# Kernel optimization log

Measured on AMD Instinct MI355X. Metric: run time of the kernel, lower is better.

## Reference

```python
import jax, jax.numpy as jnp
import numpy as np

B, T, E, H, K, V = 256, 200, 100, 128, 13, 50000


def run_lstm(x, W, U, b, reverse=False):
    """Keras LSTM with activation=relu, recurrent_activation=sigmoid.
    x: [B,T,E]; W: [E,4H]; U: [H,4H]; b: [4H]. Gate order: i, f, g, o.
    Returns hidden states [B,T,H] (time-aligned for both directions)."""
    Bn = x.shape[0]
    Hn = U.shape[0]
    xw = jnp.einsum('bte,eg->btg', x, W) + b  # precompute input projections [B,T,4H]

    def step(carry, xw_t):
        h, c = carry
        z = xw_t + h @ U
        i, f, g, o = jnp.split(z, 4, axis=-1)
        i = jax.nn.sigmoid(i)
        f = jax.nn.sigmoid(f)
        g = jax.nn.relu(g)          # activation=relu (non-cuDNN path in TF)
        c = f * c + i * g
        h = o * jax.nn.relu(c)      # output activation also relu
        return (h, c), h

    init = (jnp.zeros((Bn, Hn), x.dtype), jnp.zeros((Bn, Hn), x.dtype))
    _, hs = jax.lax.scan(step, init, jnp.swapaxes(xw, 0, 1), reverse=reverse)
    return jnp.swapaxes(hs, 0, 1)


def crf_log_likelihood(logits, labels, lens, trans):
    """tfa.text.crf_log_likelihood: score(labels) - logZ, masked by seq lens."""
    Bn, Tn, Kn = logits.shape
    t_idx = jnp.arange(Tn)
    mask = t_idx[None, :] < lens[:, None]  # [B,T]
    # unary score
    unary = jnp.take_along_axis(logits, labels[..., None], axis=-1)[..., 0]
    u_score = jnp.sum(jnp.where(mask, unary, 0.0), axis=-1)
    # transition score
    pair = trans[labels[:, :-1], labels[:, 1:]]  # [B,T-1]
    pmask = t_idx[None, 1:] < lens[:, None]
    b_score = jnp.sum(jnp.where(pmask, pair, 0.0), axis=-1)
    # forward algorithm (log-space DP over time, masked updates)
    def step(alpha, inp):
        logit_t, valid = inp  # [B,K], [B]
        new = jax.nn.logsumexp(alpha[:, :, None] + trans[None], axis=1) + logit_t
        alpha = jnp.where(valid[:, None], new, alpha)
        return alpha, None

    alpha0 = logits[:, 0, :]
    xs = (jnp.swapaxes(logits[:, 1:, :], 0, 1), jnp.swapaxes(mask[:, 1:], 0, 1))
    alpha, _ = jax.lax.scan(step, alpha0, xs)
    logZ = jax.nn.logsumexp(alpha, axis=-1)
    return u_score + b_score - logZ


def setup_inputs() -> dict:
    key = jax.random.key(0)
    ks = jax.random.split(key, 12)
    s = lambda k, shape, sc: jax.random.normal(k, shape, jnp.float32) * sc
    return {
        'text': jax.random.randint(ks[0], (B, T), 0, V).astype(jnp.int32),
        'labels': jax.random.randint(ks[1], (B, T), 0, K).astype(jnp.int32),
        'emb': s(ks[2], (V, E), 0.1),
        'Wf': s(ks[3], (E, 4 * H), 0.05),
        'Uf': s(ks[4], (H, 4 * H), 0.05),
        'bf': jnp.zeros((4 * H,), jnp.float32),
        'Wb': s(ks[5], (E, 4 * H), 0.05),
        'Ub': s(ks[6], (H, 4 * H), 0.05),
        'bb': jnp.zeros((4 * H,), jnp.float32),
        'Wd': s(ks[7], (2 * H, K), 0.05),
        'bd': jnp.zeros((K,), jnp.float32),
        'trans': jax.random.uniform(ks[8], (K, K), jnp.float32),
    }


def reference(text, labels, emb, Wf, Uf, bf, Wb, Ub, bb, Wd, bd, trans):
    lens = jnp.sum((text != 0).astype(jnp.int32), axis=-1)  # [B]
    x = emb[text]                      # embedding lookup [B,T,E]
    # dropout is identity in eval mode
    h_fwd = run_lstm(x, Wf, Uf, bf, reverse=False)
    h_bwd = run_lstm(x, Wb, Ub, bb, reverse=True)
    h = jnp.concatenate([h_fwd, h_bwd], axis=-1)  # [B,T,2H]
    logits = jax.nn.softmax(h @ Wd + bd, axis=-1)  # Dense(softmax), per source
    log_likelihood = crf_log_likelihood(logits, labels, lens, trans)
    return logits, lens, log_likelihood
```

## Files before the change

### kernel.cpp

```cpp
#include <hip/hip_runtime.h>
#include <hip/hip_bf16.h>

#define Bn 256
#define Tn 200
#define En 100
#define Hn 128
#define Kn 13
#define G4 512
#define BT 51200

typedef __attribute__((ext_vector_type(8))) __bf16 bf8_t;
typedef __attribute__((ext_vector_type(4))) float f4_t;

__device__ __forceinline__ unsigned short f2bf(float f) {
  unsigned int u = __float_as_uint(f);
  u = (u + 0x7FFFu + ((u >> 16) & 1u)) >> 16;
  return (unsigned short)u;
}
__device__ __forceinline__ float bf2f(unsigned short s) {
  return __uint_as_float(((unsigned int)s) << 16);
}
__device__ __forceinline__ float sigm(float x) { return 1.f / (1.f + __expf(-x)); }

__device__ __forceinline__ void bar_lgkm() {
  asm volatile("s_waitcnt lgkmcnt(0)" ::: "memory");
  __builtin_amdgcn_s_barrier();
  __builtin_amdgcn_sched_barrier(0);
}

__device__ __forceinline__ int gperm(int n) {
  return ((n >> 4) & 3) * 128 + ((n >> 6) << 4) + (n & 15);
}

__global__ __launch_bounds__(256) void k_prep(const int* __restrict__ text,
                                              const float* __restrict__ Wf,
                                              const float* __restrict__ Wb,
                                              const float* __restrict__ Uf,
                                              const float* __restrict__ Ub,
                                              unsigned short* __restrict__ wt,
                                              unsigned short* __restrict__ ut,
                                              int* __restrict__ lens_i,
                                              float* __restrict__ out_lens) {
  int bx = blockIdx.x;
  if (bx < 1024) {
    int idx = bx * 256 + threadIdx.x;
    int half = idx >> 17;
    int rem = idx & 131071;
    int dir = rem >> 16;
    int nk = rem & 65535;
    int n = nk >> 7, k = nk & 127;
    int mc = gperm(n);
    if (half == 0) {
      const float* W = dir ? Wb : Wf;
      wt[rem] = f2bf((k < En) ? W[k * G4 + mc] : 0.f);
    } else {
      const float* U = dir ? Ub : Uf;
      ut[rem] = f2bf(U[k * G4 + mc]);
    }
  } else {
    int wi = threadIdx.x >> 6, lane = threadIdx.x & 63;
    int b = (bx - 1024) * 4 + wi;
    int cnt = 0;
    for (int t = lane; t < Tn; t += 64) cnt += (text[b * Tn + t] != 0);
    for (int off = 32; off; off >>= 1) cnt += __shfl_down(cnt, off);
    if (lane == 0) { lens_i[b] = cnt; out_lens[b] = (float)cnt; }
  }
}

#define FR16(M) M(0,0) M(0,1) M(0,2) M(0,3) M(1,0) M(1,1) M(1,2) M(1,3) \
                M(2,0) M(2,1) M(2,2) M(2,3) M(3,0) M(3,1) M(3,2) M(3,3)

__global__ __attribute__((amdgpu_flat_work_group_size(512, 512),
                          amdgpu_waves_per_eu(1, 2)))
void k_scan(const int* __restrict__ text,
            const float* __restrict__ emb,
            const unsigned short* __restrict__ wt,
            const unsigned short* __restrict__ ut,
            const float* __restrict__ biasf,
            const float* __restrict__ biasb,
            unsigned short* __restrict__ hf,
            unsigned short* __restrict__ hb) {
  int blk = blockIdx.x;
  int dir = blk >> 6;
  int bg = blk & 63;
  int b0 = bg * 4;
  int tid = threadIdx.x;
  int w = tid >> 6, l = tid & 63;
  int lr = l & 15, lg = l >> 4;
  int jj = w * 16 + lr;
  const unsigned short* ut_d = ut + (size_t)dir * (G4 * 128);
  const unsigned short* wt_d = wt + (size_t)dir * (G4 * 128);
  const float* bias = dir ? biasb : biasf;
  unsigned short* hout = dir ? hb : hf;
  int t0 = dir ? (Tn - 1) : 0;
  int dt = dir ? -1 : 1;

#define LOADUB(nt, kk) \
  bf8_t ub_##nt##_##kk = *(const bf8_t*)(ut_d + (size_t)(w * 64 + (nt) * 16 + lr) * 128 + (kk) * 32 + lg * 8); \
  asm volatile("" : "+a"(ub_##nt##_##kk));
  FR16(LOADUB)
#undef LOADUB
#define LOADWB(nt, kk) \
  bf8_t wb_##nt##_##kk = *(const bf8_t*)(wt_d + (size_t)(w * 64 + (nt) * 16 + lr) * 128 + (kk) * 32 + lg * 8); \
  asm volatile("" : "+a"(wb_##nt##_##kk));
  FR16(LOADWB)
#undef LOADWB

  __shared__ __align__(16) char lds_all[16384 + Tn * 4 * 4];
  char* lbase = lds_all;
  int* tl = (int*)(lds_all + 16384);
  for (int i = tid; i < 4096; i += 512) ((unsigned int*)lds_all)[i] = 0;
  #pragma unroll
  for (int r = 0; r < 4; r++)
    if (tid < Tn) tl[r * Tn + tid] = text[(size_t)(b0 + r) * Tn + tid];

  float bn0 = bias[gperm(w * 64 +  0 + lr)];
  float bn1 = bias[gperm(w * 64 + 16 + lr)];
  float bn2 = bias[gperm(w * 64 + 32 + lr)];
  float bn3 = bias[gperm(w * 64 + 48 + lr)];
  f4_t bv0 = {bn0, bn0, bn0, bn0};
  f4_t bv1 = {bn1, bn1, bn1, bn1};
  f4_t bv2 = {bn2, bn2, bn2, bn2};
  f4_t bv3 = {bn3, bn3, bn3, bn3};
  f4_t z4 = {0.f, 0.f, 0.f, 0.f};

  int xrow = tid >> 7;
  int xcol = tid & 127;
  bool xon = (xcol < En);
  float v0 = 0.f, vA = 0.f, vB = 0.f;
  {
    const int* trow = text + (size_t)(b0 + xrow) * Tn;
    int k0 = trow[t0], k1 = trow[t0 + dt], k2 = trow[t0 + 2 * dt];
    if (xon) {
      v0 = emb[(size_t)k0 * En + xcol];
      vA = emb[(size_t)k1 * En + xcol];
      vB = emb[(size_t)k2 * En + xcol];
    }
  }

  int rb0 = (lr * 256 +   0 + lg * 16) ^ ((lr & 7) << 4);
  int rb1 = (lr * 256 +  64 + lg * 16) ^ ((lr & 7) << 4);
  int rb2 = (lr * 256 + 128 + lg * 16) ^ ((lr & 7) << 4);
  int rb3 = (lr * 256 + 192 + lg * 16) ^ ((lr & 7) << 4);
  int xb0 = 8192 + rb0, xb1 = 8192 + rb1, xb2 = 8192 + rb2, xb3 = 8192 + rb3;
  int wbh = (((lg * 4) * 256 + jj * 2) ^ (((lg * 4) & 7) << 4)) + 4096;
  int wbx = 8192 + (((xrow * 4) * 256 + xcol * 2) ^ (((xrow * 4) & 7) << 4));

  unsigned short* hp = hout + ((size_t)t0 * Bn + b0 + lg) * 128 + jj;
  const long long hstep = (long long)dt * Bn * 128;

  __syncthreads();
  *(unsigned short*)(lbase + wbx) = f2bf(v0);
  wbx ^= 4096;
  float c0 = 0.f;
  __syncthreads();

#define MFU(nt, kk) accU##nt = __builtin_amdgcn_mfma_f32_16x16x32_bf16(af##kk, ub_##nt##_##kk, accU##nt, 0, 0, 0);
#define MFW(nt, kk) accW##nt = __builtin_amdgcn_mfma_f32_16x16x32_bf16(ax##kk, wb_##nt##_##kk, accW##nt, 0, 0, 0);

  int t = t0;
  for (int tt = 0; tt < Tn; tt++) {
    *(unsigned short*)(lbase + wbx) = f2bf(vA);
    vA = vB;
    int tc = t + 3 * dt;
    tc = tc < 0 ? 0 : (tc > Tn - 1 ? Tn - 1 : tc);
    int tokN = tl[xrow * Tn + tc];
    vB = 0.f;
    if (xon) vB = emb[(size_t)tokN * En + xcol];
    bf8_t af0 = *(const bf8_t*)(lbase + rb0);
    bf8_t af1 = *(const bf8_t*)(lbase + rb1);
    bf8_t af2 = *(const bf8_t*)(lbase + rb2);
    bf8_t af3 = *(const bf8_t*)(lbase + rb3);
    bf8_t ax0 = *(const bf8_t*)(lbase + xb0);
    bf8_t ax1 = *(const bf8_t*)(lbase + xb1);
    bf8_t ax2 = *(const bf8_t*)(lbase + xb2);
    bf8_t ax3 = *(const bf8_t*)(lbase + xb3);
    f4_t accU0 = bv0, accU1 = bv1, accU2 = bv2, accU3 = bv3;
    f4_t accW0 = z4, accW1 = z4, accW2 = z4, accW3 = z4;
    MFU(0,0) MFU(1,0) MFU(2,0) MFU(3,0)
    MFW(0,0) MFW(1,0) MFW(2,0) MFW(3,0)
    MFU(0,1) MFU(1,1) MFU(2,1) MFU(3,1)
    MFW(0,1) MFW(1,1) MFW(2,1) MFW(3,1)
    MFU(0,2) MFU(1,2) MFU(2,2) MFU(3,2)
    MFW(0,2) MFW(1,2) MFW(2,2) MFW(3,2)
    MFU(0,3) MFU(1,3) MFU(2,3) MFU(3,3)
    MFW(0,3) MFW(1,3) MFW(2,3) MFW(3,3)
    float zi = accU0[0] + accW0[0];
    float zf = accU1[0] + accW1[0];
    float zg = accU2[0] + accW2[0];
    float zo = accU3[0] + accW3[0];
    float ig = sigm(zi);
    float fg = sigm(zf);
    float gg = fmaxf(zg, 0.f);
    c0 = fmaf(fg, c0, ig * gg);
    unsigned short hs2 = f2bf(sigm(zo) * fmaxf(c0, 0.f));
    *(unsigned short*)(lbase + wbh) = hs2;
    bar_lgkm();
    hp[0] = hs2;
    rb0 ^= 4096; rb1 ^= 4096; rb2 ^= 4096; rb3 ^= 4096;
    xb0 ^= 4096; xb1 ^= 4096; xb2 ^= 4096; xb3 ^= 4096;
    wbh ^= 4096; wbx ^= 4096;
    hp += hstep;
    t += dt;
  }
#undef MFU
#undef MFW
}

__global__ __launch_bounds__(128) void k_logits(const unsigned short* __restrict__ hf,
                                                const unsigned short* __restrict__ hb,
                                                const float* __restrict__ Wd,
                                                const float* __restrict__ bd,
                                                float* __restrict__ out) {
  __shared__ unsigned short hs[128 * 256];
  int tid = threadIdx.x;
  size_t row0 = (size_t)blockIdx.x * 128;
  #pragma unroll
  for (int it = 0; it < 16; it++) {
    int idx = it * 128 + tid;
    int r = idx >> 4, c = idx & 15;
    bf8_t vf = *(const bf8_t*)(hf + (row0 + r) * 128 + c * 8);
    bf8_t vb = *(const bf8_t*)(hb + (row0 + r) * 128 + c * 8);
    int byte = (r * 512 + c * 16) ^ ((r & 7) << 4);
    *(bf8_t*)((char*)hs + byte) = vf;
    int byte2 = (r * 512 + 256 + c * 16) ^ ((r & 7) << 4);
    *(bf8_t*)((char*)hs + byte2) = vb;
  }
  __syncthreads();
  float acc[Kn];
  #pragma unroll
  for (int jj = 0; jj < Kn; jj++) acc[jj] = bd[jj];
  int r = tid;
  #pragma unroll 4
  for (int c = 0; c < 32; c++) {
    int byte = (r * 512 + c * 16) ^ ((r & 7) << 4);
    bf8_t v = *(const bf8_t*)((const char*)hs + byte);
    #pragma unroll
    for (int e = 0; e < 8; e++) {
      float h = (float)v[e];
      int k = c * 8 + e;
      #pragma unroll
      for (int jj = 0; jj < Kn; jj++)
        acc[jj] = fmaf(h, Wd[k * Kn + jj], acc[jj]);
    }
  }
  float m = acc[0];
  #pragma unroll
  for (int jj = 1; jj < Kn; jj++) m = fmaxf(m, acc[jj]);
  float s = 0.f;
  #pragma unroll
  for (int jj = 0; jj < Kn; jj++) { acc[jj] = __expf(acc[jj] - m); s += acc[jj]; }
  float inv = 1.f / s;
  int rg = (int)row0 + tid;
  int b = rg & 255, t = rg >> 8;
  float* op = out + ((size_t)b * Tn + t) * Kn;
  #pragma unroll
  for (int jj = 0; jj < Kn; jj++) op[jj] = acc[jj] * inv;
}

__global__ __launch_bounds__(64) void k_crf(const float* __restrict__ logits,
                                            const int* __restrict__ labels,
                                            const int* __restrict__ lens_i,
                                            const float* __restrict__ trans,
                                            float* __restrict__ out_ll) {
  int b = blockIdx.x, lane = threadIdx.x;
  int len = lens_i[b];
  const float* lg = logits + (size_t)b * Tn * Kn;
  const int* lab = labels + (size_t)b * Tn;
  float sc = 0.f;
  for (int t = lane; t < Tn; t += 64) {
    if (t < len) {
      sc += lg[t * Kn + lab[t]];
      if (t >= 1) sc += trans[lab[t - 1] * Kn + lab[t]];
    }
  }
  for (int off = 32; off; off >>= 1) sc += __shfl_down(sc, off);
  bool act = lane < Kn;
  int jl = act ? lane : 0;
  float etr[Kn];
  #pragma unroll
  for (int i = 0; i < Kn; i++) etr[i] = __expf(trans[i * Kn + jl]);
  float a = act ? lg[jl] : -INFINITY;
  float lgv = (len > 1) ? lg[Kn + jl] : 0.f;
  for (int t = 1; t < len; t++) {
    float lgn = (t + 1 < len) ? lg[(t + 1) * Kn + jl] : 0.f;
    float m = a;
    for (int off = 8; off; off >>= 1) m = fmaxf(m, __shfl_xor(m, off, 16));
    float ea = __expf(a - m);
    float s = 0.f;
    #pragma unroll
    for (int i = 0; i < Kn; i++) s = fmaf(__shfl(ea, i), etr[i], s);
    float anew = m + __logf(s) + lgv;
    if (act) a = anew;
    lgv = lgn;
  }
  float m2 = a;
  for (int off = 8; off; off >>= 1) m2 = fmaxf(m2, __shfl_xor(m2, off, 16));
  float ea2 = act ? __expf(a - m2) : 0.f;
  float ssum = ea2;
  for (int off = 8; off; off >>= 1) ssum += __shfl_xor(ssum, off, 16);
  float logZ = m2 + __logf(ssum);
  if (lane == 0) out_ll[b] = sc - logZ;
}

extern "C" void kernel_launch(void* const* d_in, const int* in_sizes, int n_in,
                              void* d_out, int out_size, void* d_ws, size_t ws_size,
                              hipStream_t stream) {
  const int* text = (const int*)d_in[0];
  const int* labels = (const int*)d_in[1];
  const float* emb = (const float*)d_in[2];
  const float* Wf = (const float*)d_in[3];
  const float* Uf = (const float*)d_in[4];
  const float* bf_ = (const float*)d_in[5];
  const float* Wb = (const float*)d_in[6];
  const float* Ub = (const float*)d_in[7];
  const float* bb_ = (const float*)d_in[8];
  const float* Wd = (const float*)d_in[9];
  const float* bd = (const float*)d_in[10];
  const float* trans = (const float*)d_in[11];
  (void)in_sizes; (void)n_in; (void)out_size; (void)ws_size;

  float* out = (float*)d_out;
  float* out_logits = out;
  float* out_lens = out + (size_t)BT * Kn;
  float* out_ll = out_lens + Bn;

  char* ws = (char*)d_ws;
  size_t o = 0;
  int* lens_i = (int*)(ws + o);                o += 1024;
  unsigned short* wt = (unsigned short*)(ws + o);  o += (size_t)2 * G4 * 128 * 2;
  unsigned short* ut = (unsigned short*)(ws + o);  o += (size_t)2 * G4 * 128 * 2;
  unsigned short* hfb = (unsigned short*)(ws + o); o += (size_t)BT * Hn * 2;
  unsigned short* hbb = (unsigned short*)(ws + o); o += (size_t)BT * Hn * 2;

  hipLaunchKernelGGL(k_prep, dim3(1088), dim3(256), 0, stream,
                     text, Wf, Wb, Uf, Ub, wt, ut, lens_i, out_lens);
  hipLaunchKernelGGL(k_scan, dim3(128), dim3(512), 0, stream,
                     text, emb, wt, ut, bf_, bb_, hfb, hbb);
  hipLaunchKernelGGL(k_logits, dim3(400), dim3(128), 0, stream, hfb, hbb, Wd, bd, out_logits);
  hipLaunchKernelGGL(k_crf, dim3(Bn), dim3(64), 0, stream, out_logits, labels, lens_i, trans, out_ll);
}
```

Baseline: 319.2 us.

## Software-pipeline LSTM input projection one timestep ahead of the recurrence

The recurrent loop now computes the input-projection MFMAs (x·W plus bias) for the next timestep after the current step's h·U MFMAs, using two ping-ponged accumulator sets. The current step's gates depend only on the 16 recurrent MFMAs seeded with the precomputed projection. A prologue stages two embedding timesteps and computes the first projection, the x staging area moves to a separate LDS offset, and the loop is unrolled by two. The aim is to shorten the serial dependency chain per step and let the projection MFMAs overlap the gate math, at the cost of more accumulator registers.

```diff
diff --git a/kernel.cpp b/kernel.cpp
--- a/kernel.cpp
+++ b/kernel.cpp
@@ -122,19 +122,19 @@
   f4_t bv1 = {bn1, bn1, bn1, bn1};
   f4_t bv2 = {bn2, bn2, bn2, bn2};
   f4_t bv3 = {bn3, bn3, bn3, bn3};
-  f4_t z4 = {0.f, 0.f, 0.f, 0.f};
 
   int xrow = tid >> 7;
   int xcol = tid & 127;
   bool xon = (xcol < En);
-  float v0 = 0.f, vA = 0.f, vB = 0.f;
+  float v0 = 0.f, v1 = 0.f, vA = 0.f, vB = 0.f;
   {
     const int* trow = text + (size_t)(b0 + xrow) * Tn;
-    int k0 = trow[t0], k1 = trow[t0 + dt], k2 = trow[t0 + 2 * dt];
+    int k0 = trow[t0], k1 = trow[t0 + dt], k2 = trow[t0 + 2 * dt], k3 = trow[t0 + 3 * dt];
     if (xon) {
       v0 = emb[(size_t)k0 * En + xcol];
-      vA = emb[(size_t)k1 * En + xcol];
-      vB = emb[(size_t)k2 * En + xcol];
+      v1 = emb[(size_t)k1 * En + xcol];
+      vA = emb[(size_t)k2 * En + xcol];
+      vB = emb[(size_t)k3 * En + xcol];
     }
   }
 
@@ -142,69 +142,104 @@
   int rb1 = (lr * 256 +  64 + lg * 16) ^ ((lr & 7) << 4);
   int rb2 = (lr * 256 + 128 + lg * 16) ^ ((lr & 7) << 4);
   int rb3 = (lr * 256 + 192 + lg * 16) ^ ((lr & 7) << 4);
-  int xb0 = 8192 + rb0, xb1 = 8192 + rb1, xb2 = 8192 + rb2, xb3 = 8192 + rb3;
+  int xb0 = 12288 + rb0, xb1 = 12288 + rb1, xb2 = 12288 + rb2, xb3 = 12288 + rb3;
   int wbh = (((lg * 4) * 256 + jj * 2) ^ (((lg * 4) & 7) << 4)) + 4096;
   int wbx = 8192 + (((xrow * 4) * 256 + xcol * 2) ^ (((xrow * 4) & 7) << 4));
 
   unsigned short* hp = hout + ((size_t)t0 * Bn + b0 + lg) * 128 + jj;
   const long long hstep = (long long)dt * Bn * 128;
 
-  __syncthreads();
   *(unsigned short*)(lbase + wbx) = f2bf(v0);
-  wbx ^= 4096;
+  *(unsigned short*)(lbase + (wbx ^ 4096)) = f2bf(v1);
+  bar_lgkm();
+
+  f4_t pA0 = bv0, pA1 = bv1, pA2 = bv2, pA3 = bv3;
+  f4_t pB0, pB1, pB2, pB3;
+  {
+    bf8_t ax0 = *(const bf8_t*)(lbase + 8192 + rb0);
+    bf8_t ax1 = *(const bf8_t*)(lbase + 8192 + rb1);
+    bf8_t ax2 = *(const bf8_t*)(lbase + 8192 + rb2);
+    bf8_t ax3 = *(const bf8_t*)(lbase + 8192 + rb3);
+#define MFP(nt, kk) pA##nt = __builtin_amdgcn_mfma_f32_16x16x32_bf16(ax##kk, wb_##nt##_##kk, pA##nt, 0, 0, 0);
+    MFP(0,0) MFP(1,0) MFP(2,0) MFP(3,0)
+    MFP(0,1) MFP(1,1) MFP(2,1) MFP(3,1)
+    MFP(0,2) MFP(1,2) MFP(2,2) MFP(3,2)
+    MFP(0,3) MFP(1,3) MFP(2,3) MFP(3,3)
+#undef MFP
+  }
   float c0 = 0.f;
-  __syncthreads();
-
-#define MFU(nt, kk) accU##nt = __builtin_amdgcn_mfma_f32_16x16x32_bf16(af##kk, ub_##nt##_##kk, accU##nt, 0, 0, 0);
-#define MFW(nt, kk) accW##nt = __builtin_amdgcn_mfma_f32_16x16x32_bf16(ax##kk, wb_##nt##_##kk, accW##nt, 0, 0, 0);
-
   int t = t0;
-  for (int tt = 0; tt < Tn; tt++) {
-    *(unsigned short*)(lbase + wbx) = f2bf(vA);
-    vA = vB;
-    int tc = t + 3 * dt;
-    tc = tc < 0 ? 0 : (tc > Tn - 1 ? Tn - 1 : tc);
-    int tokN = tl[xrow * Tn + tc];
-    vB = 0.f;
-    if (xon) vB = emb[(size_t)tokN * En + xcol];
-    bf8_t af0 = *(const bf8_t*)(lbase + rb0);
-    bf8_t af1 = *(const bf8_t*)(lbase + rb1);
-    bf8_t af2 = *(const bf8_t*)(lbase + rb2);
-    bf8_t af3 = *(const bf8_t*)(lbase + rb3);
-    bf8_t ax0 = *(const bf8_t*)(lbase + xb0);
-    bf8_t ax1 = *(const bf8_t*)(lbase + xb1);
-    bf8_t ax2 = *(const bf8_t*)(lbase + xb2);
-    bf8_t ax3 = *(const bf8_t*)(lbase + xb3);
-    f4_t accU0 = bv0, accU1 = bv1, accU2 = bv2, accU3 = bv3;
-    f4_t accW0 = z4, accW1 = z4, accW2 = z4, accW3 = z4;
-    MFU(0,0) MFU(1,0) MFU(2,0) MFU(3,0)
-    MFW(0,0) MFW(1,0) MFW(2,0) MFW(3,0)
-    MFU(0,1) MFU(1,1) MFU(2,1) MFU(3,1)
-    MFW(0,1) MFW(1,1) MFW(2,1) MFW(3,1)
-    MFU(0,2) MFU(1,2) MFU(2,2) MFU(3,2)
-    MFW(0,2) MFW(1,2) MFW(2,2) MFW(3,2)
-    MFU(0,3) MFU(1,3) MFU(2,3) MFU(3,3)
-    MFW(0,3) MFW(1,3) MFW(2,3) MFW(3,3)
-    float zi = accU0[0] + accW0[0];
-    float zf = accU1[0] + accW1[0];
-    float zg = accU2[0] + accW2[0];
-    float zo = accU3[0] + accW3[0];
-    float ig = sigm(zi);
-    float fg = sigm(zf);
-    float gg = fmaxf(zg, 0.f);
-    c0 = fmaf(fg, c0, ig * gg);
-    unsigned short hs2 = f2bf(sigm(zo) * fmaxf(c0, 0.f));
-    *(unsigned short*)(lbase + wbh) = hs2;
-    bar_lgkm();
-    hp[0] = hs2;
-    rb0 ^= 4096; rb1 ^= 4096; rb2 ^= 4096; rb3 ^= 4096;
-    xb0 ^= 4096; xb1 ^= 4096; xb2 ^= 4096; xb3 ^= 4096;
-    wbh ^= 4096; wbx ^= 4096;
-    hp += hstep;
-    t += dt;
-  }
-#undef MFU
-#undef MFW
+
+#define STEPF(P, Q) { \
+    bf8_t af0 = *(const bf8_t*)(lbase + rb0); \
+    bf8_t af1 = *(const bf8_t*)(lbase + rb1); \
+    bf8_t af2 = *(const bf8_t*)(lbase + rb2); \
+    bf8_t af3 = *(const bf8_t*)(lbase + rb3); \
+     \
+    *(unsigned short*)(lbase + wbx) = f2bf(vA); \
+    vA = vB; \
+    { int tc = t + 3 * dt; tc = tc < 0 ? 0 : (tc > Tn - 1 ? Tn - 1 : tc); \
+      int tokN = tl[xrow * Tn + tc]; \
+      vB = xon ? emb[(size_t)tokN * En + xcol] : 0.f; } \
+     \
+    P##0 = __builtin_amdgcn_mfma_f32_16x16x32_bf16(af0, ub_0_0, P##0, 0, 0, 0); \
+    P##1 = __builtin_amdgcn_mfma_f32_16x16x32_bf16(af0, ub_1_0, P##1, 0, 0, 0); \
+    P##2 = __builtin_amdgcn_mfma_f32_16x16x32_bf16(af0, ub_2_0, P##2, 0, 0, 0); \
+    P##3 = __builtin_amdgcn_mfma_f32_16x16x32_bf16(af0, ub_3_0, P##3, 0, 0, 0); \
+    P##0 = __builtin_amdgcn_mfma_f32_16x16x32_bf16(af1, ub_0_1, P##0, 0, 0, 0); \
+    P##1 = __builtin_amdgcn_mfma_f32_16x16x32_bf16(af1, ub_1_1, P##1, 0, 0, 0); \
+    P##2 = __builtin_amdgcn_mfma_f32_16x16x32_bf16(af1, ub_2_1, P##2, 0, 0, 0); \
+    P##3 = __builtin_amdgcn_mfma_f32_16x16x32_bf16(af1, ub_3_1, P##3, 0, 0, 0); \
+    P##0 = __builtin_amdgcn_mfma_f32_16x16x32_bf16(af2, ub_0_2, P##0, 0, 0, 0); \
+    P##1 = __builtin_amdgcn_mfma_f32_16x16x32_bf16(af2, ub_1_2, P##1, 0, 0, 0); \
+    P##2 = __builtin_amdgcn_mfma_f32_16x16x32_bf16(af2, ub_2_2, P##2, 0, 0, 0); \
+    P##3 = __builtin_amdgcn_mfma_f32_16x16x32_bf16(af2, ub_3_2, P##3, 0, 0, 0); \
+    P##0 = __builtin_amdgcn_mfma_f32_16x16x32_bf16(af3, ub_0_3, P##0, 0, 0, 0); \
+    P##1 = __builtin_amdgcn_mfma_f32_16x16x32_bf16(af3, ub_1_3, P##1, 0, 0, 0); \
+    P##2 = __builtin_amdgcn_mfma_f32_16x16x32_bf16(af3, ub_2_3, P##2, 0, 0, 0); \
+    P##3 = __builtin_amdgcn_mfma_f32_16x16x32_bf16(af3, ub_3_3, P##3, 0, 0, 0); \
+     \
+    { bf8_t ax0 = *(const bf8_t*)(lbase + xb0); \
+      bf8_t ax1 = *(const bf8_t*)(lbase + xb1); \
+      bf8_t ax2 = *(const bf8_t*)(lbase + xb2); \
+      bf8_t ax3 = *(const bf8_t*)(lbase + xb3); \
+      Q##0 = bv0; Q##1 = bv1; Q##2 = bv2; Q##3 = bv3; \
+      Q##0 = __builtin_amdgcn_mfma_f32_16x16x32_bf16(ax0, wb_0_0, Q##0, 0, 0, 0); \
+      Q##1 = __builtin_amdgcn_mfma_f32_16x16x32_bf16(ax0, wb_1_0, Q##1, 0, 0, 0); \
+      Q##2 = __builtin_amdgcn_mfma_f32_16x16x32_bf16(ax0, wb_2_0, Q##2, 0, 0, 0); \
+      Q##3 = __builtin_amdgcn_mfma_f32_16x16x32_bf16(ax0, wb_3_0, Q##3, 0, 0, 0); \
+      Q##0 = __builtin_amdgcn_mfma_f32_16x16x32_bf16(ax1, wb_0_1, Q##0, 0, 0, 0); \
+      Q##1 = __builtin_amdgcn_mfma_f32_16x16x32_bf16(ax1, wb_1_1, Q##1, 0, 0, 0); \
+      Q##2 = __builtin_amdgcn_mfma_f32_16x16x32_bf16(ax1, wb_2_1, Q##2, 0, 0, 0); \
+      Q##3 = __builtin_amdgcn_mfma_f32_16x16x32_bf16(ax1, wb_3_1, Q##3, 0, 0, 0); \
+      Q##0 = __builtin_amdgcn_mfma_f32_16x16x32_bf16(ax2, wb_0_2, Q##0, 0, 0, 0); \
+      Q##1 = __builtin_amdgcn_mfma_f32_16x16x32_bf16(ax2, wb_1_2, Q##1, 0, 0, 0); \
+      Q##2 = __builtin_amdgcn_mfma_f32_16x16x32_bf16(ax2, wb_2_2, Q##2, 0, 0, 0); \
+      Q##3 = __builtin_amdgcn_mfma_f32_16x16x32_bf16(ax2, wb_3_2, Q##3, 0, 0, 0); \
+      Q##0 = __builtin_amdgcn_mfma_f32_16x16x32_bf16(ax3, wb_0_3, Q##0, 0, 0, 0); \
+      Q##1 = __builtin_amdgcn_mfma_f32_16x16x32_bf16(ax3, wb_1_3, Q##1, 0, 0, 0); \
+      Q##2 = __builtin_amdgcn_mfma_f32_16x16x32_bf16(ax3, wb_2_3, Q##2, 0, 0, 0); \
+      Q##3 = __builtin_amdgcn_mfma_f32_16x16x32_bf16(ax3, wb_3_3, Q##3, 0, 0, 0); } \
+     \
+    float ig = sigm(P##0[0]); \
+    float fg = sigm(P##1[0]); \
+    float gg = fmaxf(P##2[0], 0.f); \
+    c0 = fmaf(fg, c0, ig * gg); \
+    unsigned short hs2 = f2bf(sigm(P##3[0]) * fmaxf(c0, 0.f)); \
+    *(unsigned short*)(lbase + wbh) = hs2; \
+    bar_lgkm(); \
+    hp[0] = hs2; \
+    rb0 ^= 4096; rb1 ^= 4096; rb2 ^= 4096; rb3 ^= 4096; \
+    xb0 ^= 4096; xb1 ^= 4096; xb2 ^= 4096; xb3 ^= 4096; \
+    wbh ^= 4096; wbx ^= 4096; \
+    hp += hstep; \
+    t += dt; }
+
+  for (int tt = 0; tt < Tn; tt += 2) {
+    STEPF(pA, pB)
+    STEPF(pB, pA)
+  }
+#undef STEPF
 }
 
 __global__ __launch_bounds__(128) void k_logits(const unsigned short* __restrict__ hf,
```

After: 285.2 us. -10.7%, faster.
